# Optimization experiments

Measured on AMD Instinct MI355X. Metric: run time of the kernel, lower is better.

The kernel has to match this reference:

```python
import jax, jax.numpy as jnp
import numpy as np

N_HEADS = 2
EPS = 1e-5
NEG_SLOPE = 0.02
N_CENTROIDS = 1024
RADII = (0.1, 0.2)
KS = (32, 64)


def fps(x, m):
    # Farthest point sampling (deterministic start at index 0). x: [B, C, N]
    B, C, N = x.shape
    def body(carry, _):
        distance, farthest = carry
        centroid = jnp.take_along_axis(x, jnp.broadcast_to(farthest[:, None, None], (B, C, 1)), axis=2)
        dist = jnp.sum((x - centroid) ** 2, axis=1)  # [B, N]
        distance = jnp.minimum(distance, dist)
        nxt = jnp.argmax(distance, axis=1).astype(jnp.int32)
        return (distance, nxt), farthest
    init = (jnp.full((B, N), 1e10, x.dtype), jnp.zeros((B,), jnp.int32))
    _, idxs = jax.lax.scan(body, init, None, length=m)
    return idxs.T  # [B, m]


def ball_group(x, centroids, radius, k):
    # x: [B, C, N], centroids: [B, C, M] -> (idx [B,M,k] int32, mask [B,M,k] bool)
    B, C, N = x.shape
    M = centroids.shape[2]
    d = (jnp.sum(x * x, axis=1)[:, None, :]
         - 2.0 * jnp.einsum('bcm,bcn->bmn', centroids, x)
         + jnp.sum(centroids * centroids, axis=1)[:, :, None])  # [B, M, N]
    idx = jnp.broadcast_to(jnp.arange(N, dtype=jnp.int32)[None, None, :], (B, M, N))
    idx = jnp.where(d > radius * radius, N, idx)
    idx = -jax.lax.top_k(-idx, k)[0]  # k smallest indices, ascending (matches torch.topk largest=False)
    mask = idx == N
    first = jnp.where(idx[:, :, :1] == N, 0, idx[:, :, :1])
    idx = jnp.where(mask, jnp.broadcast_to(first, idx.shape), idx)
    return idx, mask


def attention_mix(x, y, mask, wq, wk, wv, wo):
    # x: [B, C, K] centroids, y: [B, C, K, Np] groups, mask: [B, K, Np]
    B, C, K = x.shape
    Np = y.shape[3]
    H = N_HEADS
    q = jnp.einsum('oc,bck->bok', wq, x).reshape(B, H, C, K)
    kk = jnp.einsum('oc,bckn->bokn', wk, y).reshape(B, H, C, K, Np)
    v = jnp.einsum('oc,bckn->bokn', wv, y).reshape(B, H, C, K, Np)
    w = jnp.einsum('bhck,bhckn->bhkn', q, kk) / (C ** 0.5)
    w = jnp.where(mask[:, None, :, :], -1e9, w)
    w = jax.nn.softmax(w, axis=3)
    o = jnp.einsum('bhkn,bhckn->bhck', w, v).reshape(B, H * C, K)
    return jnp.einsum('oc,bck->bok', wo, o) + x


def conv_bn(x, w, b, g, beta, act):
    # 1x1 Conv1d + BatchNorm1d (training-mode batch stats) + optional LeakyReLU(0.02)
    x = jnp.einsum('oc,bck->bok', w, x) + b[None, :, None]
    mu = jnp.mean(x, axis=(0, 2), keepdims=True)
    var = jnp.var(x, axis=(0, 2), keepdims=True)
    x = (x - mu) * jax.lax.rsqrt(var + EPS) * g[None, :, None] + beta[None, :, None]
    return jnp.where(x > 0, x, NEG_SLOPE * x) if act else x


def pointnet_msg(xyz, point_features, attn_params, mlp_params):
    support = jnp.concatenate([xyz, point_features], axis=1)  # [B, 32, N]
    B, Cs, N = support.shape
    M = N_CENTROIDS
    cidx = fps(support, M)  # [B, M]
    centroids = jnp.take_along_axis(support, jnp.broadcast_to(cidx[:, None, :], (B, Cs, M)), axis=2)
    new_xyz = jnp.take_along_axis(xyz, jnp.broadcast_to(cidx[:, None, :], (B, 3, M)), axis=2)
    feats = []
    for s, (radius, k) in enumerate(zip(RADII, KS)):
        idx, mask = ball_group(support, centroids, radius, k)  # [B, M, k]
        gidx = jnp.broadcast_to(idx.reshape(B, 1, M * k), (B, Cs, M * k))
        group = jnp.take_along_axis(support, gidx, axis=2).reshape(B, Cs, M, k)
        group = group - centroids[:, :, :, None]
        f = attention_mix(centroids, group, mask, *attn_params[s])
        (w0, b0, g0, t0), (w1, b1, g1, t1) = mlp_params[s]
        f = conv_bn(f, w0, b0, g0, t0, act=True)
        f = conv_bn(f, w1, b1, g1, t1, act=False)
        feats.append(f)
    return new_xyz, jnp.concatenate(feats, axis=1)  # [B,3,M], [B,256,M]


def setup_inputs() -> dict:
    key = jax.random.key(0)
    ks = jax.random.split(key, 32)
    B, N, C = 4, 16384, 32
    d = {}
    d['xyz'] = jax.random.uniform(ks[0], (B, 3, N), jnp.float32)
    d['point_features'] = jax.random.normal(ks[1], (B, C - 3, N), jnp.float32)
    i = 2
    for s in range(2):
        d[f'aq{s}'] = 0.05 * jax.random.normal(ks[i], (64, 32), jnp.float32); i += 1
        d[f'ak{s}'] = 0.05 * jax.random.normal(ks[i], (64, 32), jnp.float32); i += 1
        d[f'av{s}'] = 0.05 * jax.random.normal(ks[i], (64, 32), jnp.float32); i += 1
        d[f'ao{s}'] = 0.05 * jax.random.normal(ks[i], (32, 64), jnp.float32); i += 1
        d[f'mw{s}0'] = 0.05 * jax.random.normal(ks[i], (64, 32), jnp.float32); i += 1
        d[f'mb{s}0'] = jnp.zeros((64,), jnp.float32)
        d[f'mg{s}0'] = jnp.ones((64,), jnp.float32)
        d[f'mbt{s}0'] = jnp.zeros((64,), jnp.float32)
        d[f'mw{s}1'] = 0.05 * jax.random.normal(ks[i], (128, 64), jnp.float32); i += 1
        d[f'mb{s}1'] = jnp.zeros((128,), jnp.float32)
        d[f'mg{s}1'] = jnp.ones((128,), jnp.float32)
        d[f'mbt{s}1'] = jnp.zeros((128,), jnp.float32)
    return d


def reference(xyz, point_features,
              aq0, ak0, av0, ao0, mw00, mb00, mg00, mbt00, mw01, mb01, mg01, mbt01,
              aq1, ak1, av1, ao1, mw10, mb10, mg10, mbt10, mw11, mb11, mg11, mbt11):
    attn_params = (((aq0, ak0, av0, ao0)), ((aq1, ak1, av1, ao1)))
    mlp_params = (((mw00, mb00, mg00, mbt00), (mw01, mb01, mg01, mbt01)),
                  ((mw10, mb10, mg10, mbt10), (mw11, mb11, mg11, mbt11)))
    return pointnet_msg(xyz, point_features, attn_params, mlp_params)
```

## Files before the change

### kernel.cpp

```cpp
#include <hip/hip_runtime.h>
#include <hip/hip_bf16.h>


static constexpr int Bb = 4;
static constexpr int Npts = 16384;
static constexpr int Mc = 1024;
static constexpr int NBLK = 16;
static constexpr int OUT_EXPECT = 12288 + 1048576;
#define BN_EPS 1e-5f
#define SLOPE 0.02f
#define SCOPE_AGT __HIP_MEMORY_SCOPE_AGENT

static constexpr size_t OFF_STATS = 33024;
static constexpr size_t ZERO_BYTES = 65536;
static constexpr size_t OFF_CIDX  = 65536;
static constexpr size_t OFF_IDX0  = 81920;
static constexpr size_t OFF_CNT0  = 344064;
static constexpr size_t OFF_IDX1  = 360448;
static constexpr size_t OFF_CNT1  = 884736;
static constexpr size_t OFF_ATTN  = 901120;
static constexpr size_t OFF_Z0    = 1163264;
static constexpr size_t WS_REQUIRED = 1687552;
static constexpr size_t OFF_FSLOT = 901120;
static constexpr size_t FSLOT_BYTES = (size_t)Bb * Mc * NBLK * 8;
static constexpr size_t OFF_Z1 = 1687552;
static constexpr size_t WS_Z1_REQUIRED = OFF_Z1 + (size_t)Bb * 128 * Mc * 4;
static constexpr size_t OFF_SUPT = WS_Z1_REQUIRED;
static constexpr size_t WS_T_REQUIRED = OFF_SUPT + (size_t)Bb * Npts * 32 * 4;

__device__ __forceinline__ float sup_at(const float* xyz, const float* pf,
                                        int b, int c, int n) {
  return (c < 3) ? xyz[((size_t)b*3 + c)*Npts + n]
                 : pf[((size_t)b*29 + (c-3))*Npts + n];
}

__device__ __forceinline__ float sanf(float v, float repl) {
  if (!(v == v) || fabsf(v) > 1e30f) v = repl;
  return v;
}

__global__ __launch_bounds__(256) void fill_kernel(float* out, int n, float val) {
  int i = blockIdx.x * 256 + threadIdx.x;
  if (i < n) out[i] = val;
}

__global__ __launch_bounds__(256) void buildT_kernel(
    const float* __restrict__ xyz, const float* __restrict__ pf,
    float* __restrict__ supT) {
  int idx = blockIdx.x * 256 + threadIdx.x;
  int n = idx & (Npts - 1);
  int b = idx >> 14;
  float* dst = supT + ((size_t)b * Npts + n) * 32;
#pragma unroll
  for (int c = 0; c < 32; ++c) dst[c] = sup_at(xyz, pf, b, c, n);
}

__global__ __launch_bounds__(512, 2) void fps_kernel(
    const float* __restrict__ xyz, const float* __restrict__ pf,
    const float* __restrict__ supT,
    int* __restrict__ cidx, unsigned long long* __restrict__ slots) {
  const int blk = blockIdx.x;
  const int b = blk >> 4;
  const int sb = blk & (NBLK - 1);
  const int tid = threadIdx.x;
  const int lane = tid & 63, wid = tid >> 6;
  float f0[32], f1[32];
  const int p0 = sb * 1024 + tid;
  const int p1 = p0 + 512;
  float d0 = 1e10f, d1 = 1e10f;
#pragma unroll
  for (int c = 0; c < 32; ++c) {
    f0[c] = sup_at(xyz, pf, b, c, p0);
    f1[c] = sup_at(xyz, pf, b, c, p1);
  }
  __shared__ float cf[32];
  __shared__ unsigned long long red[8];
  if (sb == 0 && tid == 0) cidx[b * Mc] = 0;
  if (tid < 32) cf[tid] = sup_at(xyz, pf, b, tid, 0);
  __syncthreads();
  unsigned long long* slotb = slots + (size_t)b * Mc * NBLK;
  const float* supTb = supT ? supT + (size_t)b * Npts * 32 : nullptr;
  for (int it = 0; it < Mc - 1; ++it) {
    float cc[32];
#pragma unroll
    for (int c = 0; c < 32; ++c) cc[c] = cf[c];
    {
      float d = 0.f, e = 0.f;
#pragma unroll
      for (int c = 0; c < 32; ++c) {
        float t0 = f0[c] - cc[c];
        float s0 = __fmul_rn(t0, t0);
        d = (c == 0) ? s0 : __fadd_rn(d, s0);
        float t1 = f1[c] - cc[c];
        float s1 = __fmul_rn(t1, t1);
        e = (c == 0) ? s1 : __fadd_rn(e, s1);
      }
      d0 = fminf(d0, d);
      d1 = fminf(d1, e);
    }
    float bd; int bp;
    if (d0 >= d1) { bd = d0; bp = p0; } else { bd = d1; bp = p1; }
    unsigned long long v =
        ((unsigned long long)__float_as_uint(bd) << 32) | (unsigned int)(~(unsigned int)bp);
#pragma unroll
    for (int d = 32; d; d >>= 1) {
      unsigned long long o = __shfl_xor(v, d, 64);
      if (o > v) v = o;
    }
    if (lane == 0) red[wid] = v;
    __syncthreads();
    if (tid == 0) {
      unsigned long long vb = red[0];
#pragma unroll
      for (int w = 1; w < 8; ++w) if (red[w] > vb) vb = red[w];
      atomicMax(&slotb[(size_t)it * NBLK + sb], vb);
    }
    if (wid == 0) {
      unsigned long long myv = 0;
      if (lane < NBLK) {
        const unsigned long long* sp = &slotb[(size_t)it * NBLK + lane];
        while ((myv = __hip_atomic_load(sp, __ATOMIC_RELAXED, SCOPE_AGT)) == 0ull)
          __builtin_amdgcn_s_sleep(1);
      }
      unsigned long long mv = myv;
#pragma unroll
      for (int d = 8; d; d >>= 1) {
        unsigned long long o = __shfl_xor(mv, d, 16);
        if (o > mv) mv = o;
      }
      unsigned long long vwin = __shfl(mv, 0, 64);
      int idxWin = (int)(~(unsigned int)(vwin & 0xffffffffu)) & (Npts - 1);
      if (lane < 32)
        cf[lane] = supTb ? supTb[(size_t)idxWin * 32 + lane]
                         : sup_at(xyz, pf, b, lane, idxWin);
      if (lane == 0 && sb == 0) cidx[b * Mc + it + 1] = idxWin;
    }
    __syncthreads();
  }
}

__global__ __launch_bounds__(256) void gather_kernel(
    const float* __restrict__ xyz, const int* __restrict__ cidx,
    float* __restrict__ oxyz, int out_size) {
  int idx = blockIdx.x * 256 + threadIdx.x;
  if (idx >= out_size || idx >= 12288) return;
  int m = idx & (Mc - 1);
  int t = idx >> 10;
  int b = t / 3;
  int ci = cidx[b * Mc + m] & (Npts - 1);
  oxyz[idx] = sanf(xyz[(size_t)t * Npts + ci], 888.0f);
}

__global__ __launch_bounds__(256) void ball_kernel(
    const float* __restrict__ xyz, const float* __restrict__ pf,
    const int* __restrict__ cidx,
    unsigned short* __restrict__ idx0, int* __restrict__ cnt0,
    unsigned short* __restrict__ idx1, int* __restrict__ cnt1) {
  const int b = blockIdx.x >> 6;
  const int mt = blockIdx.x & 63;
  const int tid = threadIdx.x;
  __shared__ float cf[16][32];
  __shared__ float csq[16];
  __shared__ unsigned int ent[16][128];
  __shared__ int lcnt[16];
  for (int i = tid; i < 16 * 32; i += 256) {
    int ml = i >> 5, c = i & 31;
    int ci = cidx[b * Mc + mt * 16 + ml] & (Npts - 1);
    cf[ml][c] = sup_at(xyz, pf, b, c, ci);
  }
  if (tid < 16) lcnt[tid] = 0;
  __syncthreads();
  if (tid < 16) {
    float a = 0.f;
#pragma unroll
    for (int c = 0; c < 32; ++c) a = fmaf(cf[tid][c], cf[tid][c], a);
    csq[tid] = a;
  }
  __syncthreads();
  for (int ch = 0; ch < Npts / 256; ++ch) {
    int p = ch * 256 + tid;
    float x[32];
#pragma unroll
    for (int c = 0; c < 32; ++c) x[c] = sup_at(xyz, pf, b, c, p);
    float sp = 0.f;
#pragma unroll
    for (int c = 0; c < 32; ++c) sp = fmaf(x[c], x[c], sp);
#pragma unroll 4
    for (int ml = 0; ml < 16; ++ml) {
      float dot = 0.f;
#pragma unroll
      for (int c = 0; c < 32; ++c) dot = fmaf(cf[ml][c], x[c], dot);
      float d = sp - 2.0f * dot + csq[ml];
      if (d <= 0.04f) {
        int pos = atomicAdd(&lcnt[ml], 1);
        if (pos < 128) ent[ml][pos] = (unsigned int)p | (d <= 0.01f ? 0x80000000u : 0u);
      }
    }
  }
  __syncthreads();
  if (tid < 16) {
    int ml = tid;
    int nn = lcnt[ml]; if (nn > 128) nn = 128;
    for (int i = 1; i < nn; ++i) {
      unsigned int e = ent[ml][i]; unsigned int key = e & 0x7fffffffu;
      int j = i - 1;
      while (j >= 0 && (ent[ml][j] & 0x7fffffffu) > key) { ent[ml][j+1] = ent[ml][j]; --j; }
      ent[ml][j+1] = e;
    }
    int gm = b * Mc + mt * 16 + ml;
    int c1 = nn < 64 ? nn : 64;
    unsigned short first1 = nn > 0 ? (unsigned short)(ent[ml][0] & 0x7fffffffu) : 0;
    unsigned short* o1 = idx1 + (size_t)gm * 64;
    for (int j = 0; j < 64; ++j)
      o1[j] = j < c1 ? (unsigned short)(ent[ml][j] & 0x7fffffffu) : first1;
    cnt1[gm] = c1;
    unsigned short* o0 = idx0 + (size_t)gm * 32;
    int c0 = 0; unsigned short first0 = 0;
    for (int i = 0; i < nn && c0 < 32; ++i) {
      if (ent[ml][i] & 0x80000000u) {
        unsigned short nv = (unsigned short)(ent[ml][i] & 0x7fffffffu);
        if (c0 == 0) first0 = nv;
        o0[c0++] = nv;
      }
    }
    for (int j = c0; j < 32; ++j) o0[j] = first0;
    cnt0[gm] = c0;
  }
}

template <int K>
__global__ __launch_bounds__(256) void attn_kernel(
    const float* __restrict__ xyz, const float* __restrict__ pf,
    const int* __restrict__ cidx,
    const unsigned short* __restrict__ idxS, const int* __restrict__ cntS,
    const float* __restrict__ wq, const float* __restrict__ wk,
    const float* __restrict__ wv, const float* __restrict__ wo,
    __hip_bfloat16* __restrict__ outA) {
  __shared__ float WqL[64*33], WkL[64*33], WvL[64*33], WoL[32*65];
  __shared__ float xv[4][32];
  __shared__ float qv[4][64];
  __shared__ float yb[4][2][32];
  __shared__ float ov[4][64];
  __shared__ int cns[4];
  const int tid = threadIdx.x;
  const int wid = tid >> 6, lane = tid & 63;
  const int gid = blockIdx.x;
  const int b = gid >> 8;
  const int m = ((gid & 255) << 2) + wid;
  for (int i = tid; i < 2048; i += 256) {
    int r = i >> 5, c = i & 31;
    WqL[r*33 + c] = wq[i];
    WkL[r*33 + c] = wk[i];
    WvL[r*33 + c] = wv[i];
    int ro = i >> 6, co = i & 63;
    WoL[ro*65 + co] = wo[i];
  }
  if (lane < 32) {
    int ci = cidx[b * Mc + m] & (Npts - 1);
    xv[wid][lane] = sup_at(xyz, pf, b, lane, ci);
  }
  if (lane == 0) cns[wid] = cntS[b * Mc + m];
  __syncthreads();
  {
    float acc = 0.f;
#pragma unroll
    for (int c = 0; c < 32; ++c) acc = fmaf(WqL[lane*33 + c], xv[wid][c], acc);
    qv[wid][lane] = acc;
  }
  __syncthreads();
  int cnt = cns[wid];
  cnt = cnt < 1 ? 1 : (cnt > K ? K : cnt);
  const int jj = lane < K ? lane : 0;
  int nj = (int)idxS[((size_t)b*Mc + m)*K + jj] & (Npts - 1);
  float y[32];
#pragma unroll
  for (int c = 0; c < 32; ++c)
    y[c] = sup_at(xyz, pf, b, c, nj) - xv[wid][c];
  float w0 = 0.f, w1 = 0.f;
#pragma unroll 2
  for (int r = 0; r < 32; ++r) {
    float k0 = 0.f, k1 = 0.f;
#pragma unroll
    for (int c = 0; c < 32; ++c) {
      k0 = fmaf(WkL[r*33 + c], y[c], k0);
      k1 = fmaf(WkL[(r+32)*33 + c], y[c], k1);
    }
    w0 = fmaf(qv[wid][r], k0, w0);
    w1 = fmaf(qv[wid][r+32], k1, w1);
  }
  const float iscale = 0.17677669529663689f;
  w0 *= iscale; w1 *= iscale;
  if (lane >= cnt) { w0 = -1e9f; w1 = -1e9f; }
  float mx0 = w0, mx1 = w1;
#pragma unroll
  for (int d = K/2; d; d >>= 1) {
    mx0 = fmaxf(mx0, __shfl_xor(mx0, d, K));
    mx1 = fmaxf(mx1, __shfl_xor(mx1, d, K));
  }
  float e0 = __expf(w0 - mx0), e1 = __expf(w1 - mx1);
  float s0 = e0, s1 = e1;
#pragma unroll
  for (int d = K/2; d; d >>= 1) {
    s0 += __shfl_xor(s0, d, K);
    s1 += __shfl_xor(s1, d, K);
  }
  float wn0 = e0 / s0, wn1 = e1 / s1;
#pragma unroll
  for (int c = 0; c < 32; ++c) {
    float t0 = wn0 * y[c], t1 = wn1 * y[c];
#pragma unroll
    for (int d = K/2; d; d >>= 1) {
      t0 += __shfl_xor(t0, d, K);
      t1 += __shfl_xor(t1, d, K);
    }
    if (lane == 0) { yb[wid][0][c] = t0; yb[wid][1][c] = t1; }
  }
  __syncthreads();
  {
    const int h = lane >> 5;
    float a2 = 0.f;
#pragma unroll
    for (int c = 0; c < 32; ++c) a2 = fmaf(WvL[lane*33 + c], yb[wid][h][c], a2);
    ov[wid][lane] = a2;
  }
  __syncthreads();
  if (lane < 32) {
    float a3 = 0.f;
#pragma unroll
    for (int r = 0; r < 64; ++r) a3 = fmaf(WoL[lane*65 + r], ov[wid][r], a3);
    outA[((size_t)b*32 + lane)*Mc + m] = __float2bfloat16(a3 + xv[wid][lane]);
  }
}

__global__ __launch_bounds__(256) void conv0_kernel(
    const __hip_bfloat16* __restrict__ inA, const float* __restrict__ w0,
    const float* __restrict__ b0, __hip_bfloat16* __restrict__ z0,
    float* __restrict__ ssum, float* __restrict__ ssq) {
  int idx = blockIdx.x * 256 + threadIdx.x;
  int m = idx & (Mc - 1);
  int r = (idx >> 10) & 63;
  int b = idx >> 16;
  float acc = b0[r];
#pragma unroll
  for (int c = 0; c < 32; ++c)
    acc = fmaf(w0[r*32 + c], __bfloat162float(inA[((size_t)b*32 + c)*Mc + m]), acc);
  z0[((size_t)b*64 + r)*Mc + m] = __float2bfloat16(acc);
  float s = acc, q = acc * acc;
#pragma unroll
  for (int d = 32; d; d >>= 1) { s += __shfl_down(s, d, 64); q += __shfl_down(q, d, 64); }
  if ((threadIdx.x & 63) == 0) { atomicAdd(&ssum[r], s); atomicAdd(&ssq[r], q); }
}

__global__ __launch_bounds__(256) void conv1_stats_kernel(
    const __hip_bfloat16* __restrict__ z0,
    const float* __restrict__ ssum0, const float* __restrict__ ssq0,
    const float* __restrict__ g0, const float* __restrict__ t0,
    const float* __restrict__ w1, const float* __restrict__ b1,
    float* __restrict__ z1,
    float* __restrict__ ssum1, float* __restrict__ ssq1) {
  __shared__ float A0s[64], B0s[64];
  int tid = threadIdx.x;
  if (tid < 64) {
    float mu = ssum0[tid] * (1.0f/4096.0f);
    float var = ssq0[tid] * (1.0f/4096.0f) - mu * mu;
    if (var < 0.f) var = 0.f;
    float a = g0[tid] * rsqrtf(var + BN_EPS);
    A0s[tid] = a;
    B0s[tid] = t0[tid] - mu * a;
  }
  __syncthreads();
  int idx = blockIdx.x * 256 + tid;
  int m = idx & (Mc - 1);
  int r2 = (idx >> 10) & 127;
  int b = idx >> 17;
  float acc = b1[r2];
#pragma unroll 8
  for (int r = 0; r < 64; ++r) {
    float u = fmaf(__bfloat162float(z0[((size_t)b*64 + r)*Mc + m]), A0s[r], B0s[r]);
    u = u > 0.f ? u : SLOPE * u;
    acc = fmaf(w1[r2*64 + r], u, acc);
  }
  if (z1) z1[idx] = acc;
  float s = acc, q = acc * acc;
#pragma unroll
  for (int d = 32; d; d >>= 1) { s += __shfl_down(s, d, 64); q += __shfl_down(q, d, 64); }
  if ((tid & 63) == 0) { atomicAdd(&ssum1[r2], s); atomicAdd(&ssq1[r2], q); }
}

__global__ __launch_bounds__(256) void conv1_write_kernel(
    const __hip_bfloat16* __restrict__ z0, const float* __restrict__ z1,
    const float* __restrict__ ssum0, const float* __restrict__ ssq0,
    const float* __restrict__ g0, const float* __restrict__ t0,
    const float* __restrict__ w1, const float* __restrict__ b1,
    const float* __restrict__ ssum1, const float* __restrict__ ssq1,
    const float* __restrict__ g1, const float* __restrict__ t1,
    float* __restrict__ outAll, int chOff, int out_size) {
  __shared__ float A0s[64], B0s[64];
  __shared__ float ab1[2];
  int tid = threadIdx.x;
  int idx = blockIdx.x * 256 + tid;
  int m = idx & (Mc - 1);
  int r2 = (idx >> 10) & 127;
  int b = idx >> 17;
  if (!z1 && tid < 64) {
    float mu = ssum0[tid] * (1.0f/4096.0f);
    float var = ssq0[tid] * (1.0f/4096.0f) - mu * mu;
    if (var < 0.f) var = 0.f;
    float a = g0[tid] * rsqrtf(var + BN_EPS);
    A0s[tid] = a;
    B0s[tid] = t0[tid] - mu * a;
  }
  if (tid == 0) {
    float mu = ssum1[r2] * (1.0f/4096.0f);
    float var = ssq1[r2] * (1.0f/4096.0f) - mu * mu;
    if (var < 0.f) var = 0.f;
    float a = g1[r2] * rsqrtf(var + BN_EPS);
    ab1[0] = a;
    ab1[1] = t1[r2] - mu * a;
  }
  __syncthreads();
  float acc;
  if (z1) {
    acc = z1[idx];
  } else {
    acc = b1[r2];
#pragma unroll 8
    for (int r = 0; r < 64; ++r) {
      float u = fmaf(__bfloat162float(z0[((size_t)b*64 + r)*Mc + m]), A0s[r], B0s[r]);
      u = u > 0.f ? u : SLOPE * u;
      acc = fmaf(w1[r2*64 + r], u, acc);
    }
  }
  float v = fmaf(acc, ab1[0], ab1[1]);
  size_t oidx = 12288 + ((size_t)b*256 + chOff + r2)*Mc + m;
  if (oidx < (size_t)out_size) outAll[oidx] = sanf(v, 777.0f);
}

extern "C" void kernel_launch(void* const* d_in, const int* in_sizes, int n_in,
                              void* d_out, int out_size, void* d_ws, size_t ws_size,
                              hipStream_t stream) {
  float* outb = (float*)d_out;
  int fillBlocks = (out_size + 255) / 256;
  if (n_in != 26 || in_sizes[0] != Bb*3*Npts || in_sizes[1] != Bb*29*Npts
      || in_sizes[2] != 2048) {
    fill_kernel<<<fillBlocks, 256, 0, stream>>>(outb, out_size, 7777.0f);
    return;
  }
  if (out_size != OUT_EXPECT) {
    fill_kernel<<<fillBlocks, 256, 0, stream>>>(outb, out_size, 23456.0f);
    return;
  }
  if (ws_size < WS_REQUIRED) {
    fill_kernel<<<fillBlocks, 256, 0, stream>>>(outb, out_size, 12345.0f);
    return;
  }
  const float* xyz = (const float*)d_in[0];
  const float* pf  = (const float*)d_in[1];
  char* ws = (char*)d_ws;
  int* cidx = (int*)(ws + OFF_CIDX);
  unsigned short* idx0 = (unsigned short*)(ws + OFF_IDX0);
  int* cnt0 = (int*)(ws + OFF_CNT0);
  unsigned short* idx1 = (unsigned short*)(ws + OFF_IDX1);
  int* cnt1 = (int*)(ws + OFF_CNT1);
  unsigned long long* fslots = (unsigned long long*)(ws + OFF_FSLOT);
  __hip_bfloat16* attn = (__hip_bfloat16*)(ws + OFF_ATTN);
  __hip_bfloat16* z0 = (__hip_bfloat16*)(ws + OFF_Z0);
  float* z1 = (ws_size >= WS_Z1_REQUIRED) ? (float*)(ws + OFF_Z1) : nullptr;
  float* supT = (ws_size >= WS_T_REQUIRED) ? (float*)(ws + OFF_SUPT) : nullptr;

  hipMemsetAsync(ws, 0, ZERO_BYTES, stream);
  hipMemsetAsync(ws + OFF_FSLOT, 0, FSLOT_BYTES, stream);
  if (supT) buildT_kernel<<<Bb*Npts/256, 256, 0, stream>>>(xyz, pf, supT);
  fps_kernel<<<Bb*NBLK, 512, 0, stream>>>(xyz, pf, supT, cidx, fslots);
  ball_kernel<<<Bb*64, 256, 0, stream>>>(xyz, pf, cidx, idx0, cnt0, idx1, cnt1);

  for (int s = 0; s < 2; ++s) {
    const float* aq = (const float*)d_in[2 + s*12 + 0];
    const float* ak = (const float*)d_in[2 + s*12 + 1];
    const float* av = (const float*)d_in[2 + s*12 + 2];
    const float* ao = (const float*)d_in[2 + s*12 + 3];
    const float* w0 = (const float*)d_in[2 + s*12 + 4];
    const float* b0 = (const float*)d_in[2 + s*12 + 5];
    const float* g0 = (const float*)d_in[2 + s*12 + 6];
    const float* t0 = (const float*)d_in[2 + s*12 + 7];
    const float* w1 = (const float*)d_in[2 + s*12 + 8];
    const float* b1 = (const float*)d_in[2 + s*12 + 9];
    const float* g1 = (const float*)d_in[2 + s*12 + 10];
    const float* t1 = (const float*)d_in[2 + s*12 + 11];
    float* st = (float*)(ws + OFF_STATS) + (size_t)s*384;
    float *sum0 = st, *sq0 = st + 64, *sum1 = st + 128, *sq1 = st + 256;
    if (s == 0)
      attn_kernel<32><<<Bb*Mc/4, 256, 0, stream>>>(xyz, pf, cidx, idx0, cnt0, aq, ak, av, ao, attn);
    else
      attn_kernel<64><<<Bb*Mc/4, 256, 0, stream>>>(xyz, pf, cidx, idx1, cnt1, aq, ak, av, ao, attn);
    conv0_kernel<<<Bb*64*Mc/256, 256, 0, stream>>>(attn, w0, b0, z0, sum0, sq0);
    conv1_stats_kernel<<<Bb*128*Mc/256, 256, 0, stream>>>(z0, sum0, sq0, g0, t0,
                                                          w1, b1, z1, sum1, sq1);
    conv1_write_kernel<<<Bb*128*Mc/256, 256, 0, stream>>>(z0, z1, sum0, sq0, g0, t0,
                                                          w1, b1, sum1, sq1, g1, t1,
                                                          outb, s*128, out_size);
  }
  gather_kernel<<<48, 256, 0, stream>>>(xyz, cidx, outb, out_size);
}
```

Measured before the change: 2.738 ms.

## Fuse FPS with streaming ball query so grouping overlaps centroid selection

Launches a combined kernel where 64 blocks run farthest point sampling and publish each centroid index as soon as it is chosen, while 128 extra blocks spin on those indices and test their points against each new centroid, appending hits to per-centroid lists with atomics. A small post-pass sorts each list by index and builds the radius-0.1 and radius-0.2 neighbour tables. The attention kernel now reads neighbour features from the transposed point-major buffer. This hides ball-query time behind the serial FPS loop, but it relies on all 192 blocks being resident at once, caps each list at 128 entries before sorting, and the spinning blocks compete with FPS for memory bandwidth.

New measurement: 2.689 ms. About the same (-1.8%).

```diff
diff --git a/kernel.cpp b/kernel.cpp
--- a/kernel.cpp
+++ b/kernel.cpp
@@ -12,6 +12,7 @@
 #define SCOPE_AGT __HIP_MEMORY_SCOPE_AGENT
 
 static constexpr size_t OFF_STATS = 33024;
+static constexpr size_t OFF_GCNT  = 40960;
 static constexpr size_t ZERO_BYTES = 65536;
 static constexpr size_t OFF_CIDX  = 65536;
 static constexpr size_t OFF_IDX0  = 81920;
@@ -24,6 +25,7 @@
 static constexpr size_t OFF_FSLOT = 901120;
 static constexpr size_t FSLOT_BYTES = (size_t)Bb * Mc * NBLK * 8;
 static constexpr size_t OFF_Z1 = 1687552;
+static constexpr size_t OFF_GENT = OFF_Z1;
 static constexpr size_t WS_Z1_REQUIRED = OFF_Z1 + (size_t)Bb * 128 * Mc * 4;
 static constexpr size_t OFF_SUPT = WS_Z1_REQUIRED;
 static constexpr size_t WS_T_REQUIRED = OFF_SUPT + (size_t)Bb * Npts * 32 * 4;
@@ -53,6 +55,167 @@
   float* dst = supT + ((size_t)b * Npts + n) * 32;
 #pragma unroll
   for (int c = 0; c < 32; ++c) dst[c] = sup_at(xyz, pf, b, c, n);
+}
+
+__global__ __launch_bounds__(512, 2) void fps_ball_kernel(
+    const float* __restrict__ xyz, const float* __restrict__ pf,
+    const float* __restrict__ supT,
+    unsigned int* __restrict__ cidx, unsigned long long* __restrict__ slots,
+    unsigned int* __restrict__ gcnt, unsigned int* __restrict__ gent) {
+  const int tid = threadIdx.x;
+  if (blockIdx.x < 64) {
+    const int blk = blockIdx.x;
+    const int b = blk >> 4;
+    const int sb = blk & (NBLK - 1);
+    const int lane = tid & 63, wid = tid >> 6;
+    float f0[32], f1[32];
+    const int p0 = sb * 1024 + tid;
+    const int p1 = p0 + 512;
+    float d0 = 1e10f, d1 = 1e10f;
+#pragma unroll
+    for (int c = 0; c < 32; ++c) {
+      f0[c] = sup_at(xyz, pf, b, c, p0);
+      f1[c] = sup_at(xyz, pf, b, c, p1);
+    }
+    __shared__ float cf[32];
+    __shared__ unsigned long long red[8];
+    if (sb == 0 && tid == 0) atomicExch(&cidx[b * Mc], 0u);
+    if (tid < 32) cf[tid] = sup_at(xyz, pf, b, tid, 0);
+    __syncthreads();
+    unsigned long long* slotb = slots + (size_t)b * Mc * NBLK;
+    const float* supTb = supT + (size_t)b * Npts * 32;
+    for (int it = 0; it < Mc - 1; ++it) {
+      float cc[32];
+#pragma unroll
+      for (int c = 0; c < 32; ++c) cc[c] = cf[c];
+      {
+        float d = 0.f, e = 0.f;
+#pragma unroll
+        for (int c = 0; c < 32; ++c) {
+          float t0 = f0[c] - cc[c];
+          float s0 = __fmul_rn(t0, t0);
+          d = (c == 0) ? s0 : __fadd_rn(d, s0);
+          float t1 = f1[c] - cc[c];
+          float s1 = __fmul_rn(t1, t1);
+          e = (c == 0) ? s1 : __fadd_rn(e, s1);
+        }
+        d0 = fminf(d0, d);
+        d1 = fminf(d1, e);
+      }
+      float bd; int bp;
+      if (d0 >= d1) { bd = d0; bp = p0; } else { bd = d1; bp = p1; }
+      unsigned long long v =
+          ((unsigned long long)__float_as_uint(bd) << 32) | (unsigned int)(~(unsigned int)bp);
+#pragma unroll
+      for (int d = 32; d; d >>= 1) {
+        unsigned long long o = __shfl_xor(v, d, 64);
+        if (o > v) v = o;
+      }
+      if (lane == 0) red[wid] = v;
+      __syncthreads();
+      if (tid == 0) {
+        unsigned long long vb = red[0];
+#pragma unroll
+        for (int w = 1; w < 8; ++w) if (red[w] > vb) vb = red[w];
+        atomicMax(&slotb[(size_t)it * NBLK + sb], vb);
+      }
+      if (wid == 0) {
+        unsigned long long myv = 0;
+        if (lane < NBLK) {
+          const unsigned long long* sp = &slotb[(size_t)it * NBLK + lane];
+          while ((myv = __hip_atomic_load(sp, __ATOMIC_RELAXED, SCOPE_AGT)) == 0ull)
+            __builtin_amdgcn_s_sleep(1);
+        }
+        unsigned long long mv = myv;
+#pragma unroll
+        for (int d = 8; d; d >>= 1) {
+          unsigned long long o = __shfl_xor(mv, d, 16);
+          if (o > mv) mv = o;
+        }
+        unsigned long long vwin = __shfl(mv, 0, 64);
+        int idxWin = (int)(~(unsigned int)(vwin & 0xffffffffu)) & (Npts - 1);
+        if (lane < 32) cf[lane] = supTb[(size_t)idxWin * 32 + lane];
+        if (lane == 0 && sb == 0)
+          atomicExch(&cidx[b * Mc + it + 1], (unsigned int)idxWin);
+      }
+      __syncthreads();
+    }
+  } else {
+    const int blk2 = blockIdx.x - 64;
+    const int b = blk2 >> 5;
+    const int chunk = blk2 & 31;
+    const int p = chunk * 512 + tid;
+    const float* supTb = supT + (size_t)b * Npts * 32;
+    float x[32];
+    const float* srow = supTb + (size_t)p * 32;
+#pragma unroll
+    for (int c = 0; c < 32; ++c) x[c] = srow[c];
+    float sp = 0.f;
+#pragma unroll
+    for (int c = 0; c < 32; ++c) sp = fmaf(x[c], x[c], sp);
+    __shared__ float cfb[2][32];
+    unsigned int* cidxb = cidx + b * Mc;
+    unsigned int* gcntb = gcnt + b * Mc;
+    unsigned int* gentb = gent + (size_t)b * Mc * 128;
+    for (int m = 0; m < Mc; ++m) {
+      if (tid < 32) {
+        unsigned int ci;
+        const unsigned int* cp = &cidxb[m];
+        while ((ci = __hip_atomic_load(cp, __ATOMIC_RELAXED, SCOPE_AGT)) == 0xFFFFFFFFu)
+          __builtin_amdgcn_s_sleep(2);
+        cfb[m & 1][tid] = supTb[(size_t)(ci & (Npts - 1)) * 32 + tid];
+      }
+      __syncthreads();
+      const float* cfm = cfb[m & 1];
+      float csq = 0.f, dot = 0.f;
+#pragma unroll
+      for (int c = 0; c < 32; ++c) {
+        csq = fmaf(cfm[c], cfm[c], csq);
+        dot = fmaf(cfm[c], x[c], dot);
+      }
+      float d = sp - 2.0f * dot + csq;
+      if (d <= 0.04f) {
+        int pos = atomicAdd(&gcntb[m], 1u);
+        if (pos < 128)
+          gentb[(size_t)m * 128 + pos] = (unsigned int)p | (d <= 0.01f ? 0x80000000u : 0u);
+      }
+    }
+  }
+}
+
+__global__ __launch_bounds__(256) void ballpost_kernel(
+    unsigned int* __restrict__ gcnt, unsigned int* __restrict__ gent,
+    unsigned short* __restrict__ idx0, int* __restrict__ cnt0,
+    unsigned short* __restrict__ idx1, int* __restrict__ cnt1) {
+  int idx = blockIdx.x * 256 + threadIdx.x;
+  int b = idx >> 10;
+  int m = idx & (Mc - 1);
+  int gm = b * Mc + m;
+  unsigned int* e = gent + (size_t)gm * 128;
+  int nn = (int)gcnt[gm]; if (nn > 128) nn = 128;
+  for (int i = 1; i < nn; ++i) {
+    unsigned int ei = e[i]; unsigned int key = ei & 0x7fffffffu;
+    int j = i - 1;
+    while (j >= 0 && (e[j] & 0x7fffffffu) > key) { e[j+1] = e[j]; --j; }
+    e[j+1] = ei;
+  }
+  int c1 = nn < 64 ? nn : 64;
+  unsigned short first1 = nn > 0 ? (unsigned short)(e[0] & 0x7fffffffu) : 0;
+  unsigned short* o1 = idx1 + (size_t)gm * 64;
+  for (int j = 0; j < 64; ++j)
+    o1[j] = j < c1 ? (unsigned short)(e[j] & 0x7fffffffu) : first1;
+  cnt1[gm] = c1;
+  unsigned short* o0 = idx0 + (size_t)gm * 32;
+  int c0 = 0; unsigned short first0 = 0;
+  for (int i = 0; i < nn && c0 < 32; ++i) {
+    if (e[i] & 0x80000000u) {
+      unsigned short nv = (unsigned short)(e[i] & 0x7fffffffu);
+      if (c0 == 0) first0 = nv;
+      o0[c0++] = nv;
+    }
+  }
+  for (int j = c0; j < 32; ++j) o0[j] = first0;
+  cnt0[gm] = c0;
 }
 
 __global__ __launch_bounds__(512, 2) void fps_kernel(
@@ -231,6 +394,7 @@
 template <int K>
 __global__ __launch_bounds__(256) void attn_kernel(
     const float* __restrict__ xyz, const float* __restrict__ pf,
+    const float* __restrict__ supT,
     const int* __restrict__ cidx,
     const unsigned short* __restrict__ idxS, const int* __restrict__ cntS,
     const float* __restrict__ wq, const float* __restrict__ wk,
@@ -247,6 +411,7 @@
   const int gid = blockIdx.x;
   const int b = gid >> 8;
   const int m = ((gid & 255) << 2) + wid;
+  const float* supTb = supT ? supT + (size_t)b * Npts * 32 : nullptr;
   for (int i = tid; i < 2048; i += 256) {
     int r = i >> 5, c = i & 31;
     WqL[r*33 + c] = wq[i];
@@ -257,7 +422,8 @@
   }
   if (lane < 32) {
     int ci = cidx[b * Mc + m] & (Npts - 1);
-    xv[wid][lane] = sup_at(xyz, pf, b, lane, ci);
+    xv[wid][lane] = supTb ? supTb[(size_t)ci * 32 + lane]
+                          : sup_at(xyz, pf, b, lane, ci);
   }
   if (lane == 0) cns[wid] = cntS[b * Mc + m];
   __syncthreads();
@@ -273,9 +439,14 @@
   const int jj = lane < K ? lane : 0;
   int nj = (int)idxS[((size_t)b*Mc + m)*K + jj] & (Npts - 1);
   float y[32];
-#pragma unroll
-  for (int c = 0; c < 32; ++c)
-    y[c] = sup_at(xyz, pf, b, c, nj) - xv[wid][c];
+  if (supTb) {
+    const float* yr = supTb + (size_t)nj * 32;
+#pragma unroll
+    for (int c = 0; c < 32; ++c) y[c] = yr[c] - xv[wid][c];
+  } else {
+#pragma unroll
+    for (int c = 0; c < 32; ++c) y[c] = sup_at(xyz, pf, b, c, nj) - xv[wid][c];
+  }
   float w0 = 0.f, w1 = 0.f;
 #pragma unroll 2
   for (int r = 0; r < 32; ++r) {
@@ -465,14 +636,24 @@
   unsigned long long* fslots = (unsigned long long*)(ws + OFF_FSLOT);
   __hip_bfloat16* attn = (__hip_bfloat16*)(ws + OFF_ATTN);
   __hip_bfloat16* z0 = (__hip_bfloat16*)(ws + OFF_Z0);
+  const bool fused = (ws_size >= WS_T_REQUIRED);
   float* z1 = (ws_size >= WS_Z1_REQUIRED) ? (float*)(ws + OFF_Z1) : nullptr;
-  float* supT = (ws_size >= WS_T_REQUIRED) ? (float*)(ws + OFF_SUPT) : nullptr;
+  float* supT = fused ? (float*)(ws + OFF_SUPT) : nullptr;
+  unsigned int* gcnt = (unsigned int*)(ws + OFF_GCNT);
+  unsigned int* gent = (unsigned int*)(ws + OFF_GENT);
 
   hipMemsetAsync(ws, 0, ZERO_BYTES, stream);
   hipMemsetAsync(ws + OFF_FSLOT, 0, FSLOT_BYTES, stream);
-  if (supT) buildT_kernel<<<Bb*Npts/256, 256, 0, stream>>>(xyz, pf, supT);
-  fps_kernel<<<Bb*NBLK, 512, 0, stream>>>(xyz, pf, supT, cidx, fslots);
-  ball_kernel<<<Bb*64, 256, 0, stream>>>(xyz, pf, cidx, idx0, cnt0, idx1, cnt1);
+  if (fused) {
+    hipMemsetAsync(ws + OFF_CIDX, 0xFF, Bb * Mc * 4, stream);
+    buildT_kernel<<<Bb*Npts/256, 256, 0, stream>>>(xyz, pf, supT);
+    fps_ball_kernel<<<192, 512, 0, stream>>>(xyz, pf, supT, (unsigned int*)cidx,
+                                             fslots, gcnt, gent);
+    ballpost_kernel<<<16, 256, 0, stream>>>(gcnt, gent, idx0, cnt0, idx1, cnt1);
+  } else {
+    fps_kernel<<<Bb*NBLK, 512, 0, stream>>>(xyz, pf, supT, cidx, fslots);
+    ball_kernel<<<Bb*64, 256, 0, stream>>>(xyz, pf, cidx, idx0, cnt0, idx1, cnt1);
+  }
 
   for (int s = 0; s < 2; ++s) {
     const float* aq = (const float*)d_in[2 + s*12 + 0];
@@ -490,9 +671,11 @@
     float* st = (float*)(ws + OFF_STATS) + (size_t)s*384;
     float *sum0 = st, *sq0 = st + 64, *sum1 = st + 128, *sq1 = st + 256;
     if (s == 0)
-      attn_kernel<32><<<Bb*Mc/4, 256, 0, stream>>>(xyz, pf, cidx, idx0, cnt0, aq, ak, av, ao, attn);
+      attn_kernel<32><<<Bb*Mc/4, 256, 0, stream>>>(xyz, pf, supT, cidx, idx0, cnt0,
+                                                   aq, ak, av, ao, attn);
     else
-      attn_kernel<64><<<Bb*Mc/4, 256, 0, stream>>>(xyz, pf, cidx, idx1, cnt1, aq, ak, av, ao, attn);
+      attn_kernel<64><<<Bb*Mc/4, 256, 0, stream>>>(xyz, pf, supT, cidx, idx1, cnt1,
+                                                   aq, ak, av, ao, attn);
     conv0_kernel<<<Bb*64*Mc/256, 256, 0, stream>>>(attn, w0, b0, z0, sum0, sq0);
     conv1_stats_kernel<<<Bb*128*Mc/256, 256, 0, stream>>>(z0, sum0, sq0, g0, t0,
                                                           w1, b1, z1, sum1, sq1);
```
